# Kernel optimization log

Hardware: AMD Instinct MI355X
Metric: run time of the kernel (lower is better)

Reference implementation:

```python
import jax, jax.numpy as jnp
import numpy as np

N_STEPS = 7
N_TERMS = 4


def _sobel_kernel2d():
    dx = jnp.array([[-1.0, 0.0, 1.0], [-2.0, 0.0, 2.0], [-1.0, 0.0, 1.0]], dtype=jnp.float32)
    dy = jnp.array([[-1.0, -2.0, -1.0], [0.0, 0.0, 0.0], [1.0, 2.0, 1.0]], dtype=jnp.float32)
    return 0.125 * jnp.stack([dy, dx, dy, dx], 0)[:, None]  # [4,1,3,3]


def _grid_sample_bilinear(src, sx, sy):
    # src: [N,C,H,W]; sx,sy: [N,H,W] pixel coords (align_corners=False, zeros padding)
    N, C, H, W = src.shape
    x0 = jnp.floor(sx)
    y0 = jnp.floor(sy)
    wx = (sx - x0)[:, None]  # [N,1,H,W]
    wy = (sy - y0)[:, None]
    x0i = x0.astype(jnp.int32)
    y0i = y0.astype(jnp.int32)

    def gather(yi, xi):
        valid = ((xi >= 0) & (xi < W) & (yi >= 0) & (yi < H))
        xc = jnp.clip(xi, 0, W - 1)
        yc = jnp.clip(yi, 0, H - 1)
        v = jax.vmap(lambda im, y, x: im[:, y, x])(src, yc, xc)  # [N,C,H,W]
        return v * valid[:, None].astype(src.dtype)

    v00 = gather(y0i, x0i)
    v01 = gather(y0i, x0i + 1)
    v10 = gather(y0i + 1, x0i)
    v11 = gather(y0i + 1, x0i + 1)
    return (v00 * (1 - wx) * (1 - wy) + v01 * wx * (1 - wy)
            + v10 * (1 - wx) * wy + v11 * wx * wy)


def _transform(src, disp, gy, gx, H, W):
    # new pixel locations; torch normalizes with (size-1) but samples with
    # align_corners=False, net mapping: p -> p*S/(S-1) - 0.5
    py = gy + disp[:, 0]
    px = gx + disp[:, 1]
    sy = py * (H / (H - 1)) - 0.5
    sx = px * (W / (W - 1)) - 0.5
    return _grid_sample_bilinear(src, sx, sy)


def _jacobian2d(vel):
    # replicate-pad then depthwise sobel conv -> [N,2,2,H,W]
    N, _, H, W = vel.shape
    padded = jnp.pad(vel, ((0, 0), (0, 0), (1, 1), (1, 1)), mode='edge')
    jac = jax.lax.conv_general_dilated(
        padded, _sobel_kernel2d(), window_strides=(1, 1), padding='VALID',
        feature_group_count=2, dimension_numbers=('NCHW', 'OIHW', 'NCHW'))
    return jac.reshape(N, 2, 2, H, W)


def _logdet1p(jac, eps):
    # -sum_n (-eps)^n tr(J^n)/n over the 2x2 dims, per pixel -> [N,H,W]
    ld = jnp.zeros(jac.shape[:1] + jac.shape[-2:], dtype=jac.dtype)
    xn = jac
    for n in range(1, N_TERMS + 1):
        if n > 1:
            xn = jnp.einsum('nikhw,nkjhw->nijhw', xn, jac)
        tr = xn[:, 0, 0] + xn[:, 1, 1]
        ld = ld - ((-eps) ** n) * tr / n
    return ld


def _integrate(vel, logdet_jac):
    N, _, H, W = vel.shape
    gy, gx = jnp.meshgrid(jnp.arange(H, dtype=vel.dtype),
                          jnp.arange(W, dtype=vel.dtype), indexing='ij')
    eps = 2.0 ** (-N_STEPS)
    disp = eps * vel
    if logdet_jac:
        ldjac = _logdet1p(_jacobian2d(vel), eps)[:, None]  # [N,1,H,W]
    else:
        ldjac = None
    for _ in range(N_STEPS):
        disp = disp + _transform(disp, disp, gy, gx, H, W)
        if logdet_jac:
            ldjac = ldjac + _transform(ldjac, disp, gy, gx, H, W)
    return disp, ldjac


def setup_inputs() -> dict:
    key = jax.random.key(0)
    vel = jax.random.normal(key, (16, 2, 512, 512), dtype=jnp.float32)
    return {"vel": vel, "logdet_jac": 1}


def reference(vel, logdet_jac):
    return _integrate(vel, bool(logdet_jac))
```

## Files before the change

### kernel.cpp

```cpp
#include <hip/hip_runtime.h>


#define NB 16
#define HH 512
#define WW 512
#define HW (HH * WW)
#define TOT (NB * HW)
#define EPS 0.0078125f
#define DISP_ELEMS (NB * 2 * HW)
#define SC (512.0f / 511.0f)

typedef _Float16 f16;
typedef _Float16 f16x2 __attribute__((ext_vector_type(2)));

struct Samp {
    int i00, i01, i10, i11;
    float w00, w01, w10, w11;
};

__device__ __forceinline__ Samp make_samp(float sy, float sx) {
    float fy = floorf(sy), fx = floorf(sx);
    float wy = sy - fy, wx = sx - fx;
    int y0 = (int)fy, x0 = (int)fx;
    int y1 = y0 + 1, x1 = x0 + 1;
    bool xv0 = (unsigned)x0 < (unsigned)WW;
    bool xv1 = (unsigned)x1 < (unsigned)WW;
    bool yv0 = (unsigned)y0 < (unsigned)HH;
    bool yv1 = (unsigned)y1 < (unsigned)HH;
    int xc0 = min(max(x0, 0), WW - 1), xc1 = min(max(x1, 0), WW - 1);
    int yc0 = min(max(y0, 0), HH - 1), yc1 = min(max(y1, 0), HH - 1);
    Samp s;
    s.i00 = yc0 * WW + xc0; s.i01 = yc0 * WW + xc1;
    s.i10 = yc1 * WW + xc0; s.i11 = yc1 * WW + xc1;
    float omwx = 1.0f - wx, omwy = 1.0f - wy;
    s.w00 = (xv0 && yv0) ? omwx * omwy : 0.0f;
    s.w01 = (xv1 && yv0) ? wx * omwy   : 0.0f;
    s.w10 = (xv0 && yv1) ? omwx * wy   : 0.0f;
    s.w11 = (xv1 && yv1) ? wx * wy     : 0.0f;
    return s;
}

__device__ __forceinline__ int remap_idx() {
    int bid = blockIdx.x;
    int task = ((bid & 7) << 11) | (bid >> 3);
    return task * 256 + threadIdx.x;
}

__device__ __forceinline__ float rnd16(float v) { return (float)(f16)v; }

__global__ void __launch_bounds__(256) init_fused(const float* __restrict__ vel,
                                                  f16x2* __restrict__ ddst,
                                                  f16* __restrict__ ldst) {
    int idx = remap_idx();
    int n = idx >> 18;
    int rem = idx & (HW - 1);
    int y = rem >> 9, x = rem & (WW - 1);

    const float* v0 = vel + (size_t)n * 2 * HW;
    const float* v1 = v0 + HW;

    int ym = max(y - 1, 0), yp = min(y + 1, HH - 1);
    int xm = max(x - 1, 0), xp = min(x + 1, WW - 1);
    int rmm = ym * WW + xm, rm0 = ym * WW + x, rmp = ym * WW + xp;
    int r0m = y * WW + xm,  r00 = y * WW + x,  r0p = y * WW + xp;
    int rpm = yp * WW + xm, rp0 = yp * WW + x, rpp = yp * WW + xp;

    float a, b, c, d;
    {
        float tmm = v0[rmm], tm0 = v0[rm0], tmp = v0[rmp];
        float t0m = v0[r0m],                t0p = v0[r0p];
        float tpm = v0[rpm], tp0 = v0[rp0], tpp = v0[rpp];
        a = 0.125f * ((tpm + 2.0f * tp0 + tpp) - (tmm + 2.0f * tm0 + tmp));
        b = 0.125f * ((tmp + 2.0f * t0p + tpp) - (tmm + 2.0f * t0m + tpm));
    }
    {
        float tmm = v1[rmm], tm0 = v1[rm0], tmp = v1[rmp];
        float t0m = v1[r0m],                t0p = v1[r0p];
        float tpm = v1[rpm], tp0 = v1[rp0], tpp = v1[rpp];
        c = 0.125f * ((tpm + 2.0f * tp0 + tpp) - (tmm + 2.0f * tm0 + tmp));
        d = 0.125f * ((tmp + 2.0f * t0p + tpp) - (tmm + 2.0f * t0m + tpm));
    }

    float xa = a, xb = b, xc = c, xd = d;
    float ld = EPS * (xa + xd);
    float na = xa * a + xb * c, nb = xa * b + xb * d;
    float nc = xc * a + xd * c, nd = xc * b + xd * d;
    xa = na; xb = nb; xc = nc; xd = nd;
    ld -= (EPS * EPS) * (xa + xd) * 0.5f;
    na = xa * a + xb * c; nb = xa * b + xb * d;
    nc = xc * a + xd * c; nd = xc * b + xd * d;
    xa = na; xb = nb; xc = nc; xd = nd;
    ld += (EPS * EPS * EPS) * (xa + xd) * (1.0f / 3.0f);
    na = xa * a + xb * c;
    nd = xc * b + xd * d;
    ld -= (EPS * EPS * EPS * EPS) * (na + nd) * 0.25f;

    ldst[(size_t)n * HW + rem] = (f16)ld;

    float d0 = rnd16(EPS * v0[r00]);
    float d1 = rnd16(EPS * v1[r00]);

    float sy = fmaf((float)y + d0, SC, -0.5f);
    float sx = fmaf((float)x + d1, SC, -0.5f);
    Samp s = make_samp(sy, sx);

    float g00x = rnd16(EPS * v0[s.i00]), g00y = rnd16(EPS * v1[s.i00]);
    float g01x = rnd16(EPS * v0[s.i01]), g01y = rnd16(EPS * v1[s.i01]);
    float g10x = rnd16(EPS * v0[s.i10]), g10y = rnd16(EPS * v1[s.i10]);
    float g11x = rnd16(EPS * v0[s.i11]), g11y = rnd16(EPS * v1[s.i11]);

    float nd0 = d0 + s.w00 * g00x + s.w01 * g01x + s.w10 * g10x + s.w11 * g11x;
    float nd1 = d1 + s.w00 * g00y + s.w01 * g01y + s.w10 * g10y + s.w11 * g11y;

    f16x2 w; w.x = (f16)nd0; w.y = (f16)nd1;
    ddst[(size_t)n * HW + rem] = w;
}

__global__ void __launch_bounds__(256) step_full(const f16x2* __restrict__ dsrc,
                                                 const f16* __restrict__ lsrc,
                                                 f16x2* __restrict__ ddst,
                                                 f16* __restrict__ ldst) {
    int idx = remap_idx();
    int n = idx >> 18;
    int rem = idx & (HW - 1);
    int y = rem >> 9, x = rem & (WW - 1);

    const f16x2* dp = dsrc + (size_t)n * HW;
    const f16*   lp = lsrc + (size_t)n * HW;

    f16x2 dv = dp[rem];
    f16   lv = lp[rem];
    float d0 = (float)dv.x, d1 = (float)dv.y;

    float sy = fmaf((float)y + d0, SC, -0.5f);
    float sx = fmaf((float)x + d1, SC, -0.5f);
    Samp s = make_samp(sy, sx);

    f16x2 g00 = dp[s.i00], g01 = dp[s.i01], g10 = dp[s.i10], g11 = dp[s.i11];
    f16   h00 = lp[s.i00], h01 = lp[s.i01], h10 = lp[s.i10], h11 = lp[s.i11];

    float nd0 = d0 + s.w00 * (float)g00.x + s.w01 * (float)g01.x
                   + s.w10 * (float)g10.x + s.w11 * (float)g11.x;
    float nd1 = d1 + s.w00 * (float)g00.y + s.w01 * (float)g01.y
                   + s.w10 * (float)g10.y + s.w11 * (float)g11.y;
    float nl  = (float)lv + s.w00 * (float)h00 + s.w01 * (float)h01
                          + s.w10 * (float)h10 + s.w11 * (float)h11;

    f16x2 w; w.x = (f16)nd0; w.y = (f16)nd1;
    ddst[(size_t)n * HW + rem] = w;
    ldst[(size_t)n * HW + rem] = (f16)nl;
}

__global__ void __launch_bounds__(256) step_final(const f16x2* __restrict__ dsrc,
                                                  const f16* __restrict__ lsrc,
                                                  float* __restrict__ doutp,
                                                  float* __restrict__ loutp) {
    int idx = remap_idx();
    int n = idx >> 18;
    int rem = idx & (HW - 1);
    int y = rem >> 9, x = rem & (WW - 1);

    const f16x2* dp = dsrc + (size_t)n * HW;
    const f16*   lp = lsrc + (size_t)n * HW;

    f16x2 dv = dp[rem];
    f16   lv = lp[rem];
    float d0 = (float)dv.x, d1 = (float)dv.y;

    float sy = fmaf((float)y + d0, SC, -0.5f);
    float sx = fmaf((float)x + d1, SC, -0.5f);
    Samp s = make_samp(sy, sx);

    float nl = (float)lv + s.w00 * (float)lp[s.i00] + s.w01 * (float)lp[s.i01]
                         + s.w10 * (float)lp[s.i10] + s.w11 * (float)lp[s.i11];

    float* pd = doutp + (size_t)n * 2 * HW;
    pd[rem]      = d0;
    pd[HW + rem] = d1;
    loutp[(size_t)n * HW + rem] = nl;
}

extern "C" void kernel_launch(void* const* d_in, const int* in_sizes, int n_in,
                              void* d_out, int out_size, void* d_ws, size_t ws_size,
                              hipStream_t stream) {
    const float* vel = (const float*)d_in[0];
    float* out = (float*)d_out;

    char* wsb = (char*)d_ws;
    f16x2* dB = (f16x2*)wsb;
    f16x2* dC = (f16x2*)(wsb + (size_t)16 * 1024 * 1024);
    f16*   lB = (f16*)  (wsb + (size_t)32 * 1024 * 1024);
    f16*   lA = (f16*)  (wsb + (size_t)40 * 1024 * 1024);

    dim3 grid(TOT / 256), block(256);

    init_fused<<<grid, block, 0, stream>>>(vel, dC, lB);
    step_full<<<grid, block, 0, stream>>>(dC, lB, dB, lA);
    step_full<<<grid, block, 0, stream>>>(dB, lA, dC, lB);
    step_full<<<grid, block, 0, stream>>>(dC, lB, dB, lA);
    step_full<<<grid, block, 0, stream>>>(dB, lA, dC, lB);
    step_full<<<grid, block, 0, stream>>>(dC, lB, dB, lA);
    step_full<<<grid, block, 0, stream>>>(dB, lA, dC, lB);
    step_final<<<grid, block, 0, stream>>>(dC, lB, out, out + DISP_ELEMS);
}
```

Before: 127.9 us.

## Interleave displacement and logdet into packed half4 records for single gathers

Result: no change. 130.2 us (+1.9%).

```diff
diff --git a/kernel.cpp b/kernel.cpp
--- a/kernel.cpp
+++ b/kernel.cpp
@@ -11,7 +11,7 @@
 #define SC (512.0f / 511.0f)
 
 typedef _Float16 f16;
-typedef _Float16 f16x2 __attribute__((ext_vector_type(2)));
+typedef _Float16 f16x4 __attribute__((ext_vector_type(4)));
 
 struct Samp {
     int i00, i01, i10, i11;
@@ -49,8 +49,7 @@
 __device__ __forceinline__ float rnd16(float v) { return (float)(f16)v; }
 
 __global__ void __launch_bounds__(256) init_fused(const float* __restrict__ vel,
-                                                  f16x2* __restrict__ ddst,
-                                                  f16* __restrict__ ldst) {
+                                                  f16x4* __restrict__ rdst) {
     int idx = remap_idx();
     int n = idx >> 18;
     int rem = idx & (HW - 1);
@@ -95,8 +94,6 @@
     nd = xc * b + xd * d;
     ld -= (EPS * EPS * EPS * EPS) * (na + nd) * 0.25f;
 
-    ldst[(size_t)n * HW + rem] = (f16)ld;
-
     float d0 = rnd16(EPS * v0[r00]);
     float d1 = rnd16(EPS * v1[r00]);
 
@@ -112,47 +109,42 @@
     float nd0 = d0 + s.w00 * g00x + s.w01 * g01x + s.w10 * g10x + s.w11 * g11x;
     float nd1 = d1 + s.w00 * g00y + s.w01 * g01y + s.w10 * g10y + s.w11 * g11y;
 
-    f16x2 w; w.x = (f16)nd0; w.y = (f16)nd1;
-    ddst[(size_t)n * HW + rem] = w;
+    f16x4 rec;
+    rec.x = (f16)nd0; rec.y = (f16)nd1; rec.z = (f16)ld; rec.w = (f16)0.0f;
+    rdst[(size_t)n * HW + rem] = rec;
 }
 
-__global__ void __launch_bounds__(256) step_full(const f16x2* __restrict__ dsrc,
-                                                 const f16* __restrict__ lsrc,
-                                                 f16x2* __restrict__ ddst,
-                                                 f16* __restrict__ ldst) {
+__global__ void __launch_bounds__(256) step_full(const f16x4* __restrict__ rsrc,
+                                                 f16x4* __restrict__ rdst) {
     int idx = remap_idx();
     int n = idx >> 18;
     int rem = idx & (HW - 1);
     int y = rem >> 9, x = rem & (WW - 1);
 
-    const f16x2* dp = dsrc + (size_t)n * HW;
-    const f16*   lp = lsrc + (size_t)n * HW;
+    const f16x4* rp = rsrc + (size_t)n * HW;
 
-    f16x2 dv = dp[rem];
-    f16   lv = lp[rem];
-    float d0 = (float)dv.x, d1 = (float)dv.y;
+    f16x4 rv = rp[rem];
+    float d0 = (float)rv.x, d1 = (float)rv.y, l = (float)rv.z;
 
     float sy = fmaf((float)y + d0, SC, -0.5f);
     float sx = fmaf((float)x + d1, SC, -0.5f);
     Samp s = make_samp(sy, sx);
 
-    f16x2 g00 = dp[s.i00], g01 = dp[s.i01], g10 = dp[s.i10], g11 = dp[s.i11];
-    f16   h00 = lp[s.i00], h01 = lp[s.i01], h10 = lp[s.i10], h11 = lp[s.i11];
+    f16x4 g00 = rp[s.i00], g01 = rp[s.i01], g10 = rp[s.i10], g11 = rp[s.i11];
 
     float nd0 = d0 + s.w00 * (float)g00.x + s.w01 * (float)g01.x
                    + s.w10 * (float)g10.x + s.w11 * (float)g11.x;
     float nd1 = d1 + s.w00 * (float)g00.y + s.w01 * (float)g01.y
                    + s.w10 * (float)g10.y + s.w11 * (float)g11.y;
-    float nl  = (float)lv + s.w00 * (float)h00 + s.w01 * (float)h01
-                          + s.w10 * (float)h10 + s.w11 * (float)h11;
+    float nl  = l  + s.w00 * (float)g00.z + s.w01 * (float)g01.z
+                   + s.w10 * (float)g10.z + s.w11 * (float)g11.z;
 
-    f16x2 w; w.x = (f16)nd0; w.y = (f16)nd1;
-    ddst[(size_t)n * HW + rem] = w;
-    ldst[(size_t)n * HW + rem] = (f16)nl;
+    f16x4 w;
+    w.x = (f16)nd0; w.y = (f16)nd1; w.z = (f16)nl; w.w = (f16)0.0f;
+    rdst[(size_t)n * HW + rem] = w;
 }
 
-__global__ void __launch_bounds__(256) step_final(const f16x2* __restrict__ dsrc,
-                                                  const f16* __restrict__ lsrc,
+__global__ void __launch_bounds__(256) step_final(const f16x4* __restrict__ rsrc,
                                                   float* __restrict__ doutp,
                                                   float* __restrict__ loutp) {
     int idx = remap_idx();
@@ -160,19 +152,19 @@
     int rem = idx & (HW - 1);
     int y = rem >> 9, x = rem & (WW - 1);
 
-    const f16x2* dp = dsrc + (size_t)n * HW;
-    const f16*   lp = lsrc + (size_t)n * HW;
+    const f16x4* rp = rsrc + (size_t)n * HW;
 
-    f16x2 dv = dp[rem];
-    f16   lv = lp[rem];
-    float d0 = (float)dv.x, d1 = (float)dv.y;
+    f16x4 rv = rp[rem];
+    float d0 = (float)rv.x, d1 = (float)rv.y, l = (float)rv.z;
 
     float sy = fmaf((float)y + d0, SC, -0.5f);
     float sx = fmaf((float)x + d1, SC, -0.5f);
     Samp s = make_samp(sy, sx);
 
-    float nl = (float)lv + s.w00 * (float)lp[s.i00] + s.w01 * (float)lp[s.i01]
-                         + s.w10 * (float)lp[s.i10] + s.w11 * (float)lp[s.i11];
+    f16x4 g00 = rp[s.i00], g01 = rp[s.i01], g10 = rp[s.i10], g11 = rp[s.i11];
+
+    float nl = l + s.w00 * (float)g00.z + s.w01 * (float)g01.z
+                 + s.w10 * (float)g10.z + s.w11 * (float)g11.z;
 
     float* pd = doutp + (size_t)n * 2 * HW;
     pd[rem]      = d0;
@@ -186,20 +178,17 @@
     const float* vel = (const float*)d_in[0];
     float* out = (float*)d_out;
 
-    char* wsb = (char*)d_ws;
-    f16x2* dB = (f16x2*)wsb;
-    f16x2* dC = (f16x2*)(wsb + (size_t)16 * 1024 * 1024);
-    f16*   lB = (f16*)  (wsb + (size_t)32 * 1024 * 1024);
-    f16*   lA = (f16*)  (wsb + (size_t)40 * 1024 * 1024);
+    f16x4* rA = (f16x4*)d_out;
+    f16x4* rB = (f16x4*)d_ws;
 
     dim3 grid(TOT / 256), block(256);
 
-    init_fused<<<grid, block, 0, stream>>>(vel, dC, lB);
-    step_full<<<grid, block, 0, stream>>>(dC, lB, dB, lA);
-    step_full<<<grid, block, 0, stream>>>(dB, lA, dC, lB);
-    step_full<<<grid, block, 0, stream>>>(dC, lB, dB, lA);
-    step_full<<<grid, block, 0, stream>>>(dB, lA, dC, lB);
-    step_full<<<grid, block, 0, stream>>>(dC, lB, dB, lA);
-    step_full<<<grid, block, 0, stream>>>(dB, lA, dC, lB);
-    step_final<<<grid, block, 0, stream>>>(dC, lB, out, out + DISP_ELEMS);
+    init_fused<<<grid, block, 0, stream>>>(vel, rB);
+    step_full<<<grid, block, 0, stream>>>(rB, rA);
+    step_full<<<grid, block, 0, stream>>>(rA, rB);
+    step_full<<<grid, block, 0, stream>>>(rB, rA);
+    step_full<<<grid, block, 0, stream>>>(rA, rB);
+    step_full<<<grid, block, 0, stream>>>(rB, rA);
+    step_full<<<grid, block, 0, stream>>>(rA, rB);
+    step_final<<<grid, block, 0, stream>>>(rB, out, out + DISP_ELEMS);
 }
```
